# Optimization experiments

Measured on AMD Instinct MI355X. Metric: run time of the kernel, lower is better.

## Reference

```python
import jax, jax.numpy as jnp
import numpy as np

S, B, H = 2048, 32, 1024

def setup_inputs() -> dict:
    key = jax.random.key(0)
    ks = jax.random.split(key, 5)
    hidden = jax.random.normal(ks[0], (B, H), dtype=jnp.float32)
    encoder_outputs = jax.random.normal(ks[1], (S, B, H), dtype=jnp.float32)
    source_lengths = jax.random.randint(ks[2], (B,), 1, S + 1, dtype=jnp.int32)
    attn_w = jax.random.normal(ks[3], (H, 2 * H), dtype=jnp.float32) / np.sqrt(2 * H)
    attn_b = jnp.zeros((H,), dtype=jnp.float32)
    v = jax.random.uniform(ks[4], (H,), dtype=jnp.float32)
    return {"hidden": hidden, "encoder_outputs": encoder_outputs,
            "source_lengths": source_lengths, "attn_w": attn_w,
            "attn_b": attn_b, "v": v}

def reference(hidden, encoder_outputs, source_lengths, attn_w, attn_b, v):
    s, b, h = encoder_outputs.shape
    # Broadcast decoder hidden over source positions: (S,B,H)
    hid = jnp.broadcast_to(hidden[None, :, :], (s, b, h))
    cat = jnp.concatenate([hid, encoder_outputs], axis=2)          # (S,B,2H)
    energy = jnp.tanh(jnp.einsum('sbk,hk->sbh', cat, attn_w) + attn_b)  # (S,B,H)
    scores = jnp.einsum('sbh,h->bs', energy, v)                     # (B,S)
    mask = jnp.arange(s)[None, :] < source_lengths[:, None]         # (B,S)
    scores = jnp.where(mask, scores, jnp.float32(-1e10))
    attention_weights = jax.nn.softmax(scores, axis=1)              # (B,S)
    context = jnp.einsum('bs,sbh->bh', attention_weights, encoder_outputs)
    return context, attention_weights
```

## Files before the change

### kernel.cpp

```cpp
#include <hip/hip_runtime.h>

#define S_DIM 2048
#define B_DIM 32
#define H_DIM 1024
#define ROWS  (S_DIM * B_DIM)

typedef __attribute__((ext_vector_type(4))) float    f32x4;
typedef __attribute__((ext_vector_type(8))) _Float16 f16x8;


__device__ __forceinline__ unsigned short f16_bits(float f) {
  union { _Float16 h; unsigned short u; } cv;
  cv.h = (_Float16)f;
  return cv.u;
}

__device__ __forceinline__ float fast_tanh(float x) {
  x = fminf(15.0f, fmaxf(-15.0f, x));
  float z = __expf(-2.0f * x);
  return (1.0f - z) * __builtin_amdgcn_rcpf(1.0f + z);
}

__device__ __forceinline__ void load_lds16(const void* g, void* l) {
  __builtin_amdgcn_global_load_lds(
      (const __attribute__((address_space(1))) unsigned int*)g,
      (__attribute__((address_space(3))) unsigned int*)l, 16, 0, 0);
}

__global__ void convT_kernel(const float* __restrict__ enc,
                             unsigned short* __restrict__ Ep) {
  int step = blockIdx.x, t = blockIdx.y, tid = threadIdx.x;
  const float* src = enc + (size_t)t * 128 * H_DIM + step * 32;
  unsigned short* dst = Ep + ((size_t)t * 32 + step) * 512 * 8;
#pragma unroll
  for (int c = 0; c < 4; ++c) {
    int q = c * 256 + tid;
    int r = q >> 3, kq = q & 7;
    f32x4 x = *(const f32x4*)(src + (size_t)r * H_DIM + kq * 4);
    ushort4 o;
    o.x = f16_bits(x.x); o.y = f16_bits(x.y);
    o.z = f16_bits(x.z); o.w = f16_bits(x.w);
    int p = (r << 2) | ((kq >> 1) ^ ((r >> 2) & 3));
    *(ushort4*)(dst + p * 8 + (kq & 1) * 4) = o;
  }
}

__global__ void hidproj_kernel(const float* __restrict__ hidden,
                               const float* __restrict__ attn_w,
                               const float* __restrict__ attn_b,
                               float* __restrict__ hp) {
  int tid = threadIdx.x;
  int hl  = tid >> 4;
  int kp  = tid & 15;
  int h   = blockIdx.x * 16 + hl;
  const f32x4* wrow = (const f32x4*)(attn_w + (size_t)h * (2 * H_DIM)) + kp * 16;
  f32x4 w[16];
#pragma unroll
  for (int j = 0; j < 16; ++j) w[j] = wrow[j];
  float bias = attn_b[h];
  for (int b = 0; b < B_DIM; ++b) {
    const f32x4* xrow = (const f32x4*)(hidden + (size_t)b * H_DIM) + kp * 16;
    float s = 0.f;
#pragma unroll
    for (int j = 0; j < 16; ++j) {
      f32x4 x = xrow[j];
      s = fmaf(w[j].x, x.x, s); s = fmaf(w[j].y, x.y, s);
      s = fmaf(w[j].z, x.z, s); s = fmaf(w[j].w, x.w, s);
    }
    s += __shfl_xor(s, 1); s += __shfl_xor(s, 2);
    s += __shfl_xor(s, 4); s += __shfl_xor(s, 8);
    if (kp == 0) hp[(size_t)b * H_DIM + h] = s + bias;
  }
}

__global__ void packW2_kernel(const float* __restrict__ attn_w,
                              unsigned short* __restrict__ Bp) {
  int c2 = blockIdx.x * 256 + threadIdx.x;
  int ps   = c2 & 3;
  int n    = (c2 >> 2) & 127;
  int step = (c2 >> 9) & 31;
  int g    = c2 >> 14;
  int sub  = ps ^ ((n >> 2) & 3);
  int h    = g * 128 + n;
  int k    = step * 32 + sub * 8;
  const float* src = attn_w + (size_t)h * (2 * H_DIM) + H_DIM + k;
  f32x4 a = *(const f32x4*)src;
  f32x4 b = *(const f32x4*)(src + 4);
  ushort4 lo, hi;
  lo.x = f16_bits(a.x); lo.y = f16_bits(a.y); lo.z = f16_bits(a.z); lo.w = f16_bits(a.w);
  hi.x = f16_bits(b.x); hi.y = f16_bits(b.y); hi.z = f16_bits(b.z); hi.w = f16_bits(b.w);
  *(ushort4*)(Bp + (size_t)c2 * 8)     = lo;
  *(ushort4*)(Bp + (size_t)c2 * 8 + 4) = hi;
}

__global__ __launch_bounds__(256, 4)
void gemm_scores_kernel(const unsigned short* __restrict__ Ep,
                        const unsigned short* __restrict__ Bp,
                        const float* __restrict__ hp,
                        const float* __restrict__ v,
                        float* __restrict__ scores) {
  __shared__ __align__(16) unsigned short As[512 * 8];
  __shared__ __align__(16) unsigned short Bs[512 * 8];
  const int tid  = threadIdx.x;
  const int lane = tid & 63;
  const int wid  = tid >> 6;
  const int wm   = wid >> 1;
  const int wn   = wid & 1;
  const int m16  = lane & 15;
  const int quad = lane >> 4;
  const int bid  = blockIdx.x;
  const int xcd  = bid & 7;
  const int slot = bid >> 3;
  const int t    = xcd * 64 + (slot >> 3);
  const int g    = slot & 7;

  int aoff[4], boff[4];
#pragma unroll
  for (int f = 0; f < 4; ++f) {
    int r = wm * 64 + f * 16 + m16;
    aoff[f] = ((r << 2) | (quad ^ ((r >> 2) & 3))) * 8;
    int n = wn * 64 + f * 16 + m16;
    boff[f] = ((n << 2) | (quad ^ ((n >> 2) & 3))) * 8;
  }

  f32x4 acc[4][4];
#pragma unroll
  for (int i = 0; i < 4; ++i)
#pragma unroll
    for (int j = 0; j < 4; ++j) acc[i][j] = (f32x4){0.f, 0.f, 0.f, 0.f};

  const unsigned short* aBase = Ep + (size_t)t * 32 * 4096;
  const unsigned short* bBase = Bp + (size_t)g * 32 * 4096;

  for (int step = 0; step < 32; ++step) {
    const unsigned short* aS = aBase + (size_t)step * 4096;
    const unsigned short* bS = bBase + (size_t)step * 4096;
    load_lds16(aS + (size_t)tid * 8,         As + tid * 8);
    load_lds16(aS + (size_t)(256 + tid) * 8, As + (256 + tid) * 8);
    load_lds16(bS + (size_t)tid * 8,         Bs + tid * 8);
    load_lds16(bS + (size_t)(256 + tid) * 8, Bs + (256 + tid) * 8);
    __syncthreads();

    f16x8 af[4], bfr[4];
#pragma unroll
    for (int f = 0; f < 4; ++f) af[f]  = *(const f16x8*)&As[aoff[f]];
#pragma unroll
    for (int f = 0; f < 4; ++f) bfr[f] = *(const f16x8*)&Bs[boff[f]];
#pragma unroll
    for (int mf = 0; mf < 4; ++mf)
#pragma unroll
      for (int nf = 0; nf < 4; ++nf)
        acc[mf][nf] = __builtin_amdgcn_mfma_f32_16x16x32_f16(
            af[mf], bfr[nf], acc[mf][nf], 0, 0, 0);
    __syncthreads();
  }

  const int row0 = t * 128, n0 = g * 128;
#pragma unroll
  for (int mf = 0; mf < 4; ++mf) {
#pragma unroll
    for (int reg = 0; reg < 4; ++reg) {
      int row_g = row0 + wm * 64 + mf * 16 + quad * 4 + reg;
      int b     = row_g & 31;
      int s     = row_g >> 5;
      float psum = 0.f;
#pragma unroll
      for (int nf = 0; nf < 4; ++nf) {
        int col = n0 + wn * 64 + nf * 16 + m16;
        float e = acc[mf][nf][reg] + hp[b * H_DIM + col];
        e = fast_tanh(e);
        psum = fmaf(e, v[col], psum);
      }
      psum += __shfl_xor(psum, 1);
      psum += __shfl_xor(psum, 2);
      psum += __shfl_xor(psum, 4);
      psum += __shfl_xor(psum, 8);
      if (m16 == 0) atomicAdd(&scores[b * S_DIM + s], psum);
    }
  }
}

__global__ void softmax_kernel(const float* __restrict__ scores,
                               const int* __restrict__ lens,
                               float* __restrict__ wout) {
  int b = blockIdx.x, tid = threadIdx.x;
  int len = lens[b];
  float vals[8];
  float m = -3.0e38f;
#pragma unroll
  for (int i = 0; i < 8; ++i) {
    int s = i * 256 + tid;
    float x = scores[b * S_DIM + s];
    vals[i] = (s < len) ? x : -3.0e38f;
    m = fmaxf(m, vals[i]);
  }
#pragma unroll
  for (int off = 32; off > 0; off >>= 1) m = fmaxf(m, __shfl_xor(m, off));
  __shared__ float redm[4], reds[4];
  int wid = tid >> 6, lane = tid & 63;
  if (lane == 0) redm[wid] = m;
  __syncthreads();
  m = fmaxf(fmaxf(redm[0], redm[1]), fmaxf(redm[2], redm[3]));

  float e[8];
  float sum = 0.f;
#pragma unroll
  for (int i = 0; i < 8; ++i) {
    int s = i * 256 + tid;
    e[i] = (s < len) ? __expf(vals[i] - m) : 0.f;
    sum += e[i];
  }
#pragma unroll
  for (int off = 32; off > 0; off >>= 1) sum += __shfl_xor(sum, off);
  if (lane == 0) reds[wid] = sum;
  __syncthreads();
  sum = reds[0] + reds[1] + reds[2] + reds[3];
  float inv = 1.0f / sum;
#pragma unroll
  for (int i = 0; i < 8; ++i)
    wout[b * S_DIM + i * 256 + tid] = e[i] * inv;
}

__global__ void context_kernel(const unsigned short* __restrict__ Ep,
                               const float* __restrict__ wts,
                               const int* __restrict__ lens,
                               float* __restrict__ ctx) {
  int sc = blockIdx.x;
  int b0 = blockIdx.y * 2;
  int tid = threadIdx.x;
  int bb = tid >> 7;
  int c  = tid & 127;
  int b  = b0 + bb;
  int len = lens[b];
  int s0 = sc * 64;
  if (s0 >= len) return;
  int cnt = min(64, len - s0);
  int step = c >> 2, sub = c & 3;
  int hb = step * 32 + sub * 8;
  float acc[8] = {0.f, 0.f, 0.f, 0.f, 0.f, 0.f, 0.f, 0.f};
  const float* wrow = wts + (size_t)b * S_DIM + s0;
  for (int i = 0; i < cnt; ++i) {
    int s = s0 + i;
    float w = wrow[i];
    int R = s * 32 + b;
    int t = R >> 7, r = R & 127;
    size_t chunk = ((size_t)t * 32 + step) * 512 + (r << 2) + (sub ^ ((r >> 2) & 3));
    f16x8 e = *(const f16x8*)(Ep + chunk * 8);
#pragma unroll
    for (int j = 0; j < 8; ++j) acc[j] = fmaf(w, (float)e[j], acc[j]);
  }
  float* dst = ctx + (size_t)b * H_DIM + hb;
#pragma unroll
  for (int j = 0; j < 8; ++j) atomicAdd(dst + j, acc[j]);
}

extern "C" void kernel_launch(void* const* d_in, const int* in_sizes, int n_in,
                              void* d_out, int out_size, void* d_ws, size_t ws_size,
                              hipStream_t stream) {
  const float* hidden = (const float*)d_in[0];
  const float* enc    = (const float*)d_in[1];
  const int*   lens   = (const int*)d_in[2];
  const float* attn_w = (const float*)d_in[3];
  const float* attn_b = (const float*)d_in[4];
  const float* v      = (const float*)d_in[5];

  float* out_ctx = (float*)d_out;
  float* out_w   = (float*)d_out + B_DIM * H_DIM;

  char* p = (char*)d_ws;
  unsigned short* Ep = (unsigned short*)p; p += (size_t)ROWS * H_DIM * 2;
  float* scores = (float*)p;               p += (size_t)B_DIM * S_DIM * 4;
  float* hp     = (float*)p;               p += (size_t)B_DIM * H_DIM * 4;
  unsigned short* Bp = (unsigned short*)p;

  hipMemsetAsync(scores, 0, (size_t)B_DIM * S_DIM * sizeof(float), stream);
  hipMemsetAsync(out_ctx, 0, (size_t)B_DIM * H_DIM * sizeof(float), stream);

  hipLaunchKernelGGL(convT_kernel, dim3(32, ROWS / 128), dim3(256), 0, stream,
                     enc, Ep);
  hipLaunchKernelGGL(hidproj_kernel, dim3(H_DIM / 16), dim3(256), 0, stream,
                     hidden, attn_w, attn_b, hp);
  hipLaunchKernelGGL(packW2_kernel, dim3(512), dim3(256), 0, stream,
                     attn_w, Bp);
  hipLaunchKernelGGL(gemm_scores_kernel, dim3(4096), dim3(256), 0, stream,
                     Ep, Bp, hp, v, scores);
  hipLaunchKernelGGL(softmax_kernel, dim3(B_DIM), dim3(256), 0, stream,
                     scores, lens, out_w);
  hipLaunchKernelGGL(context_kernel, dim3(S_DIM / 64, B_DIM / 2), dim3(256),
                     0, stream, Ep, out_w, lens, out_ctx);
}
```

Measured before the change: 702.2 us.

## Double GEMM K-step to 64 with XOR-swizzled layout and fuse prep kernels

Changes the packed fp16 layout of encoder outputs and weights to 64-wide K chunks with an 8-way XOR swizzle, so the GEMM runs 16 K-steps of two MFMA sub-steps each. This halves the number of barrier pairs and LDS load rounds per tile. The hidden projection, weight packing and both memsets are merged into one prep kernel to cut launch overhead. LDS use per block doubles, which may reduce occupancy, and the context kernel's indexing is updated to read the new layout.

```diff
diff --git a/kernel.cpp b/kernel.cpp
--- a/kernel.cpp
+++ b/kernel.cpp
@@ -30,67 +30,77 @@
 __global__ void convT_kernel(const float* __restrict__ enc,
                              unsigned short* __restrict__ Ep) {
   int step = blockIdx.x, t = blockIdx.y, tid = threadIdx.x;
-  const float* src = enc + (size_t)t * 128 * H_DIM + step * 32;
-  unsigned short* dst = Ep + ((size_t)t * 32 + step) * 512 * 8;
+  const float* src = enc + (size_t)t * 128 * H_DIM + step * 64;
+  unsigned short* dst = Ep + (((size_t)t * 16 + step) * 1024) * 8;
 #pragma unroll
   for (int c = 0; c < 4; ++c) {
     int q = c * 256 + tid;
-    int r = q >> 3, kq = q & 7;
-    f32x4 x = *(const f32x4*)(src + (size_t)r * H_DIM + kq * 4);
-    ushort4 o;
-    o.x = f16_bits(x.x); o.y = f16_bits(x.y);
-    o.z = f16_bits(x.z); o.w = f16_bits(x.w);
-    int p = (r << 2) | ((kq >> 1) ^ ((r >> 2) & 3));
-    *(ushort4*)(dst + p * 8 + (kq & 1) * 4) = o;
-  }
-}
-
-__global__ void hidproj_kernel(const float* __restrict__ hidden,
-                               const float* __restrict__ attn_w,
-                               const float* __restrict__ attn_b,
-                               float* __restrict__ hp) {
-  int tid = threadIdx.x;
-  int hl  = tid >> 4;
-  int kp  = tid & 15;
-  int h   = blockIdx.x * 16 + hl;
-  const f32x4* wrow = (const f32x4*)(attn_w + (size_t)h * (2 * H_DIM)) + kp * 16;
-  f32x4 w[16];
-#pragma unroll
-  for (int j = 0; j < 16; ++j) w[j] = wrow[j];
-  float bias = attn_b[h];
-  for (int b = 0; b < B_DIM; ++b) {
-    const f32x4* xrow = (const f32x4*)(hidden + (size_t)b * H_DIM) + kp * 16;
-    float s = 0.f;
-#pragma unroll
-    for (int j = 0; j < 16; ++j) {
-      f32x4 x = xrow[j];
-      s = fmaf(w[j].x, x.x, s); s = fmaf(w[j].y, x.y, s);
-      s = fmaf(w[j].z, x.z, s); s = fmaf(w[j].w, x.w, s);
+    int r = q >> 3, slot = q & 7;
+    int sub = slot ^ (r & 7);
+    const float* s = src + (size_t)r * H_DIM + sub * 8;
+    f32x4 a = *(const f32x4*)s;
+    f32x4 b = *(const f32x4*)(s + 4);
+    ushort4 lo, hi;
+    lo.x = f16_bits(a.x); lo.y = f16_bits(a.y); lo.z = f16_bits(a.z); lo.w = f16_bits(a.w);
+    hi.x = f16_bits(b.x); hi.y = f16_bits(b.y); hi.z = f16_bits(b.z); hi.w = f16_bits(b.w);
+    *(ushort4*)(dst + q * 8)     = lo;
+    *(ushort4*)(dst + q * 8 + 4) = hi;
+  }
+}
+
+__global__ void prep_kernel(const float* __restrict__ hidden,
+                            const float* __restrict__ attn_w,
+                            const float* __restrict__ attn_b,
+                            float* __restrict__ hp,
+                            unsigned short* __restrict__ Bp,
+                            float* __restrict__ scores,
+                            float* __restrict__ ctx) {
+  int bid = blockIdx.x, tid = threadIdx.x;
+  if (bid < 64) {
+    int hl = tid >> 4;
+    int kp = tid & 15;
+    int h  = bid * 16 + hl;
+    const f32x4* wrow = (const f32x4*)(attn_w + (size_t)h * (2 * H_DIM)) + kp * 16;
+    f32x4 w[16];
+#pragma unroll
+    for (int j = 0; j < 16; ++j) w[j] = wrow[j];
+    float bias = attn_b[h];
+    for (int b = 0; b < B_DIM; ++b) {
+      const f32x4* xrow = (const f32x4*)(hidden + (size_t)b * H_DIM) + kp * 16;
+      float s = 0.f;
+#pragma unroll
+      for (int j = 0; j < 16; ++j) {
+        f32x4 x = xrow[j];
+        s = fmaf(w[j].x, x.x, s); s = fmaf(w[j].y, x.y, s);
+        s = fmaf(w[j].z, x.z, s); s = fmaf(w[j].w, x.w, s);
+      }
+      s += __shfl_xor(s, 1); s += __shfl_xor(s, 2);
+      s += __shfl_xor(s, 4); s += __shfl_xor(s, 8);
+      if (kp == 0) hp[(size_t)b * H_DIM + h] = s + bias;
     }
-    s += __shfl_xor(s, 1); s += __shfl_xor(s, 2);
-    s += __shfl_xor(s, 4); s += __shfl_xor(s, 8);
-    if (kp == 0) hp[(size_t)b * H_DIM + h] = s + bias;
-  }
-}
-
-__global__ void packW2_kernel(const float* __restrict__ attn_w,
-                              unsigned short* __restrict__ Bp) {
-  int c2 = blockIdx.x * 256 + threadIdx.x;
-  int ps   = c2 & 3;
-  int n    = (c2 >> 2) & 127;
-  int step = (c2 >> 9) & 31;
-  int g    = c2 >> 14;
-  int sub  = ps ^ ((n >> 2) & 3);
-  int h    = g * 128 + n;
-  int k    = step * 32 + sub * 8;
-  const float* src = attn_w + (size_t)h * (2 * H_DIM) + H_DIM + k;
-  f32x4 a = *(const f32x4*)src;
-  f32x4 b = *(const f32x4*)(src + 4);
-  ushort4 lo, hi;
-  lo.x = f16_bits(a.x); lo.y = f16_bits(a.y); lo.z = f16_bits(a.z); lo.w = f16_bits(a.w);
-  hi.x = f16_bits(b.x); hi.y = f16_bits(b.y); hi.z = f16_bits(b.z); hi.w = f16_bits(b.w);
-  *(ushort4*)(Bp + (size_t)c2 * 8)     = lo;
-  *(ushort4*)(Bp + (size_t)c2 * 8 + 4) = hi;
+  } else if (bid < 576) {
+    int id = (bid - 64) * 256 + tid;
+    int slot = id & 7;
+    int n    = (id >> 3) & 127;
+    int step = (id >> 10) & 15;
+    int g    = id >> 14;
+    int sub  = slot ^ (n & 7);
+    int h    = g * 128 + n;
+    const float* src = attn_w + (size_t)h * (2 * H_DIM) + H_DIM + step * 64 + sub * 8;
+    f32x4 a = *(const f32x4*)src;
+    f32x4 b = *(const f32x4*)(src + 4);
+    ushort4 lo, hi;
+    lo.x = f16_bits(a.x); lo.y = f16_bits(a.y); lo.z = f16_bits(a.z); lo.w = f16_bits(a.w);
+    hi.x = f16_bits(b.x); hi.y = f16_bits(b.y); hi.z = f16_bits(b.z); hi.w = f16_bits(b.w);
+    *(ushort4*)(Bp + (size_t)id * 8)     = lo;
+    *(ushort4*)(Bp + (size_t)id * 8 + 4) = hi;
+  } else if (bid < 640) {
+    int idx = (bid - 576) * 256 + tid;
+    *(f32x4*)(scores + (size_t)idx * 4) = (f32x4){0.f, 0.f, 0.f, 0.f};
+  } else {
+    int idx = (bid - 640) * 256 + tid;
+    *(f32x4*)(ctx + (size_t)idx * 4) = (f32x4){0.f, 0.f, 0.f, 0.f};
+  }
 }
 
 __global__ __launch_bounds__(256, 4)
@@ -99,8 +109,8 @@
                         const float* __restrict__ hp,
                         const float* __restrict__ v,
                         float* __restrict__ scores) {
-  __shared__ __align__(16) unsigned short As[512 * 8];
-  __shared__ __align__(16) unsigned short Bs[512 * 8];
+  __shared__ __align__(16) unsigned short As[1024 * 8];
+  __shared__ __align__(16) unsigned short Bs[1024 * 8];
   const int tid  = threadIdx.x;
   const int lane = tid & 63;
   const int wid  = tid >> 6;
@@ -108,50 +118,54 @@
   const int wn   = wid & 1;
   const int m16  = lane & 15;
   const int quad = lane >> 4;
+  const int rx   = m16 & 7;
   const int bid  = blockIdx.x;
   const int xcd  = bid & 7;
   const int slot = bid >> 3;
   const int t    = xcd * 64 + (slot >> 3);
   const int g    = slot & 7;
 
-  int aoff[4], boff[4];
-#pragma unroll
-  for (int f = 0; f < 4; ++f) {
-    int r = wm * 64 + f * 16 + m16;
-    aoff[f] = ((r << 2) | (quad ^ ((r >> 2) & 3))) * 8;
-    int n = wn * 64 + f * 16 + m16;
-    boff[f] = ((n << 2) | (quad ^ ((n >> 2) & 3))) * 8;
-  }
-
   f32x4 acc[4][4];
 #pragma unroll
   for (int i = 0; i < 4; ++i)
 #pragma unroll
     for (int j = 0; j < 4; ++j) acc[i][j] = (f32x4){0.f, 0.f, 0.f, 0.f};
 
-  const unsigned short* aBase = Ep + (size_t)t * 32 * 4096;
-  const unsigned short* bBase = Bp + (size_t)g * 32 * 4096;
-
-  for (int step = 0; step < 32; ++step) {
-    const unsigned short* aS = aBase + (size_t)step * 4096;
-    const unsigned short* bS = bBase + (size_t)step * 4096;
-    load_lds16(aS + (size_t)tid * 8,         As + tid * 8);
-    load_lds16(aS + (size_t)(256 + tid) * 8, As + (256 + tid) * 8);
-    load_lds16(bS + (size_t)tid * 8,         Bs + tid * 8);
-    load_lds16(bS + (size_t)(256 + tid) * 8, Bs + (256 + tid) * 8);
+  const unsigned short* aBase = Ep + (size_t)t * 16 * 8192;
+  const unsigned short* bBase = Bp + (size_t)g * 16 * 8192;
+
+  for (int step = 0; step < 16; ++step) {
+    const unsigned short* aS = aBase + (size_t)step * 8192;
+    const unsigned short* bS = bBase + (size_t)step * 8192;
+#pragma unroll
+    for (int c = 0; c < 4; ++c) {
+      int q = c * 256 + tid;
+      load_lds16(aS + (size_t)q * 8, As + q * 8);
+      load_lds16(bS + (size_t)q * 8, Bs + q * 8);
+    }
     __syncthreads();
 
-    f16x8 af[4], bfr[4];
-#pragma unroll
-    for (int f = 0; f < 4; ++f) af[f]  = *(const f16x8*)&As[aoff[f]];
-#pragma unroll
-    for (int f = 0; f < 4; ++f) bfr[f] = *(const f16x8*)&Bs[boff[f]];
-#pragma unroll
-    for (int mf = 0; mf < 4; ++mf)
-#pragma unroll
-      for (int nf = 0; nf < 4; ++nf)
-        acc[mf][nf] = __builtin_amdgcn_mfma_f32_16x16x32_f16(
-            af[mf], bfr[nf], acc[mf][nf], 0, 0, 0);
+#pragma unroll
+    for (int ko = 0; ko < 2; ++ko) {
+      int sl = (ko * 4 + quad) ^ rx;
+      f16x8 af[4], bfr[4];
+#pragma unroll
+      for (int f = 0; f < 4; ++f) {
+        int r = wm * 64 + f * 16 + m16;
+        af[f] = *(const f16x8*)&As[r * 64 + sl * 8];
+      }
+#pragma unroll
+      for (int f = 0; f < 4; ++f) {
+        int n = wn * 64 + f * 16 + m16;
+        bfr[f] = *(const f16x8*)&Bs[n * 64 + sl * 8];
+      }
+#pragma unroll
+      for (int mf = 0; mf < 4; ++mf)
+#pragma unroll
+        for (int nf = 0; nf < 4; ++nf)
+          acc[mf][nf] = __builtin_amdgcn_mfma_f32_16x16x32_f16(
+              af[mf], bfr[nf], acc[mf][nf], 0, 0, 0);
+    }
     __syncthreads();
   }
 
@@ -235,16 +249,17 @@
   int s0 = sc * 64;
   if (s0 >= len) return;
   int cnt = min(64, len - s0);
-  int step = c >> 2, sub = c & 3;
-  int hb = step * 32 + sub * 8;
+  int step = c >> 3, sub = c & 7;
+  int slot = sub ^ (b & 7);
+  int hb = step * 64 + sub * 8;
   float acc[8] = {0.f, 0.f, 0.f, 0.f, 0.f, 0.f, 0.f, 0.f};
   const float* wrow = wts + (size_t)b * S_DIM + s0;
   for (int i = 0; i < cnt; ++i) {
     int s = s0 + i;
     float w = wrow[i];
-    int R = s * 32 + b;
-    int t = R >> 7, r = R & 127;
-    size_t chunk = ((size_t)t * 32 + step) * 512 + (r << 2) + (sub ^ ((r >> 2) & 3));
+    int t = s >> 2;
+    int r = (s & 3) * 32 + b;
+    size_t chunk = ((size_t)t * 16 + step) * 1024 + r * 8 + slot;
     f16x8 e = *(const f16x8*)(Ep + chunk * 8);
 #pragma unroll
     for (int j = 0; j < 8; ++j) acc[j] = fmaf(w, (float)e[j], acc[j]);
@@ -273,15 +288,10 @@
   float* hp     = (float*)p;               p += (size_t)B_DIM * H_DIM * 4;
   unsigned short* Bp = (unsigned short*)p;
 
-  hipMemsetAsync(scores, 0, (size_t)B_DIM * S_DIM * sizeof(float), stream);
-  hipMemsetAsync(out_ctx, 0, (size_t)B_DIM * H_DIM * sizeof(float), stream);
-
-  hipLaunchKernelGGL(convT_kernel, dim3(32, ROWS / 128), dim3(256), 0, stream,
+  hipLaunchKernelGGL(convT_kernel, dim3(16, ROWS / 128), dim3(256), 0, stream,
                      enc, Ep);
-  hipLaunchKernelGGL(hidproj_kernel, dim3(H_DIM / 16), dim3(256), 0, stream,
-                     hidden, attn_w, attn_b, hp);
-  hipLaunchKernelGGL(packW2_kernel, dim3(512), dim3(256), 0, stream,
-                     attn_w, Bp);
+  hipLaunchKernelGGL(prep_kernel, dim3(672), dim3(256), 0, stream,
+                     hidden, attn_w, attn_b, hp, Bp, scores, out_ctx);
   hipLaunchKernelGGL(gemm_scores_kernel, dim3(4096), dim3(256), 0, stream,
                      Ep, Bp, hp, v, scores);
   hipLaunchKernelGGL(softmax_kernel, dim3(B_DIM), dim3(256), 0, stream,
```

New measurement: 663.8 us. -5.5%, faster.
